# Performance work log

Hardware: AMD Instinct MI355X
Metric: run time of the kernel (lower is better)

The kernel has to match this reference:

```python
import jax, jax.numpy as jnp
import numpy as np

D_MODEL = 4096
D_FF = 11008

def _dequant_matmul(x, w_int, s):
    # x: [N, in], w_int: [out, in] int, s: [out, 1] -> [N, out]
    w = w_int.astype(jnp.float32) * s  # dequantized weight [out, in]
    return x @ w.T

def setup_inputs() -> dict:
    key = jax.random.key(0)
    ks = jax.random.split(key, 7)
    x = jax.random.normal(ks[0], (4, 2048, D_MODEL), dtype=jnp.float32)
    gate_w = jax.random.randint(ks[1], (D_FF, D_MODEL), -128, 128, dtype=jnp.int32)
    up_w = jax.random.randint(ks[2], (D_FF, D_MODEL), -128, 128, dtype=jnp.int32)
    down_w = jax.random.randint(ks[3], (D_MODEL, D_FF), -128, 128, dtype=jnp.int32)
    gate_s = jax.random.uniform(ks[4], (D_FF, 1), dtype=jnp.float32) * 0.01
    up_s = jax.random.uniform(ks[5], (D_FF, 1), dtype=jnp.float32) * 0.01
    down_s = jax.random.uniform(ks[6], (D_MODEL, 1), dtype=jnp.float32) * 0.01
    return {"x": x, "gate_w": gate_w, "gate_s": gate_s, "up_w": up_w,
            "up_s": up_s, "down_w": down_w, "down_s": down_s}

def reference(x, gate_w, gate_s, up_w, up_s, down_w, down_s):
    batch, seq_len, hidden = x.shape
    x_flat = x.reshape(-1, hidden).astype(jnp.float32)
    gate = _dequant_matmul(x_flat, gate_w, gate_s)
    up = _dequant_matmul(x_flat, up_w, up_s)
    h = jax.nn.silu(gate) * up
    out = _dequant_matmul(h, down_w, down_s)
    return out.astype(x.dtype).reshape(batch, seq_len, hidden)
```

## Files before the change

### kernel.cpp

```cpp
#include <hip/hip_runtime.h>


typedef __attribute__((ext_vector_type(8))) __bf16 bf16x8;
typedef __attribute__((ext_vector_type(4))) float f32x4;
typedef __attribute__((ext_vector_type(8))) unsigned short ushort8;
typedef __attribute__((ext_vector_type(4))) int i32x4;

#define D_MODEL 4096
#define D_FF    11008
#define NTOK    8192

static __device__ __forceinline__ unsigned short f32_to_bf16(float f) {
    union { float f; unsigned u; } v; v.f = f;
    unsigned r = v.u + 0x7fffu + ((v.u >> 16) & 1u);
    return (unsigned short)(r >> 16);
}
static __device__ __forceinline__ float bf16_to_f32(unsigned short s) {
    union { unsigned u; float f; } v; v.u = ((unsigned)s) << 16;
    return v.f;
}
static __device__ __forceinline__ void gload_lds16(const void* g, void* l) {
    __builtin_amdgcn_global_load_lds(
        (const __attribute__((address_space(1))) void*)g,
        (__attribute__((address_space(3))) void*)l, 16, 0, 0);
}

__global__ __launch_bounds__(256)
void pack_w_kernel(const int* __restrict__ w, signed char* __restrict__ out,
                   long long total)
{
    long long i = ((long long)blockIdx.x * 256 + threadIdx.x) * 8;
    if (i >= total) return;
    int4 w0 = *(const int4*)(w + i);
    int4 w1 = *(const int4*)(w + i + 4);
    union { signed char c[8]; unsigned long long u; } r;
    r.c[0] = (signed char)w0.x; r.c[1] = (signed char)w0.y;
    r.c[2] = (signed char)w0.z; r.c[3] = (signed char)w0.w;
    r.c[4] = (signed char)w1.x; r.c[5] = (signed char)w1.y;
    r.c[6] = (signed char)w1.z; r.c[7] = (signed char)w1.w;
    *(unsigned long long*)(out + i) = r.u;
}

__global__ __launch_bounds__(256)
void dequant_w_kernel(const int* __restrict__ w, const float* __restrict__ s,
                      unsigned short* __restrict__ out, int cols, long long total)
{
    long long i = ((long long)blockIdx.x * 256 + threadIdx.x) * 8;
    if (i >= total) return;
    float sc = s[(int)(i / cols)];
    int4 w0 = *(const int4*)(w + i);
    int4 w1 = *(const int4*)(w + i + 4);
    ushort8 r;
    r[0] = f32_to_bf16((float)w0.x * sc);
    r[1] = f32_to_bf16((float)w0.y * sc);
    r[2] = f32_to_bf16((float)w0.z * sc);
    r[3] = f32_to_bf16((float)w0.w * sc);
    r[4] = f32_to_bf16((float)w1.x * sc);
    r[5] = f32_to_bf16((float)w1.y * sc);
    r[6] = f32_to_bf16((float)w1.z * sc);
    r[7] = f32_to_bf16((float)w1.w * sc);
    *(ushort8*)(out + i) = r;
}

__global__ __launch_bounds__(256)
void quant_x_kernel(const float* __restrict__ x, signed char* __restrict__ xq,
                    float* __restrict__ xs)
{
    __shared__ float red[4];
    const int row = blockIdx.x;
    const int t   = threadIdx.x;
    const float* xr = x + (size_t)row * D_MODEL;
    float4 v0 = *(const float4*)(xr + t * 16);
    float4 v1 = *(const float4*)(xr + t * 16 + 4);
    float4 v2 = *(const float4*)(xr + t * 16 + 8);
    float4 v3 = *(const float4*)(xr + t * 16 + 12);
    float m = fabsf(v0.x);
    m = fmaxf(m, fabsf(v0.y)); m = fmaxf(m, fabsf(v0.z)); m = fmaxf(m, fabsf(v0.w));
    m = fmaxf(m, fabsf(v1.x)); m = fmaxf(m, fabsf(v1.y)); m = fmaxf(m, fabsf(v1.z)); m = fmaxf(m, fabsf(v1.w));
    m = fmaxf(m, fabsf(v2.x)); m = fmaxf(m, fabsf(v2.y)); m = fmaxf(m, fabsf(v2.z)); m = fmaxf(m, fabsf(v2.w));
    m = fmaxf(m, fabsf(v3.x)); m = fmaxf(m, fabsf(v3.y)); m = fmaxf(m, fabsf(v3.z)); m = fmaxf(m, fabsf(v3.w));
    #pragma unroll
    for (int o = 32; o > 0; o >>= 1) m = fmaxf(m, __shfl_xor(m, o));
    if ((t & 63) == 0) red[t >> 6] = m;
    __syncthreads();
    m = fmaxf(fmaxf(red[0], red[1]), fmaxf(red[2], red[3]));
    m = fmaxf(m, 1e-20f);
    const float inv = 127.0f / m;
    if (t == 0) xs[row] = m / 127.0f;
    union { signed char c[16]; int4 i; } r;
    #pragma unroll
    for (int j = 0; j < 4; ++j) {
        float4 v = (j == 0) ? v0 : (j == 1) ? v1 : (j == 2) ? v2 : v3;
        r.c[j*4+0] = (signed char)(int)rintf(fminf(fmaxf(v.x*inv,-127.f),127.f));
        r.c[j*4+1] = (signed char)(int)rintf(fminf(fmaxf(v.y*inv,-127.f),127.f));
        r.c[j*4+2] = (signed char)(int)rintf(fminf(fmaxf(v.z*inv,-127.f),127.f));
        r.c[j*4+3] = (signed char)(int)rintf(fminf(fmaxf(v.w*inv,-127.f),127.f));
    }
    *(int4*)(xq + (size_t)row * D_MODEL + t * 16) = r.i;
}

template<int MODE>
__global__ __launch_bounds__(512, 2)
void gemm_i8(const signed char* __restrict__ A,
             const signed char* __restrict__ B,
             unsigned short* __restrict__ C,
             const unsigned short* __restrict__ gateb,
             const float* __restrict__ xs,
             const float* __restrict__ cs,
             int M, int N, int K)
{
    extern __shared__ char smem[];
    const int tid = threadIdx.x;
    const int l   = tid & 63;
    const int w   = tid >> 6;
    const int wm  = w >> 2;
    const int wn  = w & 3;

    const int nbx  = gridDim.x;
    const int nwg  = nbx * gridDim.y;
    const int orig = blockIdx.y * nbx + blockIdx.x;
    const int cpx  = nwg >> 3;
    const int swz  = (orig & 7) * cpx + (orig >> 3);
    const int bn = swz % nbx, bm = swz / nbx;
    const int m0 = bm * 256, n0 = bn * 256;

    const int st_r = tid >> 2;
    const int st_c = ((tid & 3) ^ ((st_r >> 1) & 3)) << 4;
    const signed char* gA = A + (size_t)(m0 + st_r) * K + st_c;
    const signed char* gB = B + (size_t)(n0 + st_r) * K + st_c;
    const size_t ld128 = (size_t)128 * K;

    const int s4v = l >> 4;
    const int rA = wm * 128 + (l & 15);
    const int rB = wn * 64  + (l & 15);
    const int offA = rA * 64 + ((s4v << 4) ^ (((rA >> 1) & 3) << 4));
    const int offB = 16384 + rB * 64 + ((s4v << 4) ^ (((rB >> 1) & 3) << 4));

    i32x4 acc[8][4] = {};
    i32x4 af[4], bfr[4];

#define SBAR()  __builtin_amdgcn_sched_barrier(0)
#define BAR()   __builtin_amdgcn_s_barrier()
#define VM4()   asm volatile("s_waitcnt vmcnt(4)" ::: "memory")

#define ST_A8(SS, NXT) do { \
    const signed char* p_ = gA + ((size_t)(SS) << 6); \
    gload_lds16(p_,         smem + (NXT) + (tid & 0xFFC0 ? 0 : 0) + (w << 10)); \
    gload_lds16(p_ + ld128, smem + (NXT) + 8192 + (w << 10)); } while (0)
#define ST_B8(SS, NXT) do { \
    const signed char* p_ = gB + ((size_t)(SS) << 6); \
    gload_lds16(p_,         smem + (NXT) + 16384 + (w << 10)); \
    gload_lds16(p_ + ld128, smem + (NXT) + 16384 + 8192 + (w << 10)); } while (0)

#define MFMA16_I8(MB) do { \
    _Pragma("unroll") \
    for (int mi_ = 0; mi_ < 4; ++mi_) { \
        _Pragma("unroll") \
        for (int ni_ = 0; ni_ < 4; ++ni_) { \
            acc[(MB) + mi_][ni_] = __builtin_amdgcn_mfma_i32_16x16x64_i8( \
                af[mi_], bfr[ni_], acc[(MB) + mi_][ni_], 0, 0, 0); \
        } } } while (0)

#define STEP8(CUR, NXT, SS) do { \
    af[0]  = *(const i32x4*)(smem + (CUR) + offA); \
    af[1]  = *(const i32x4*)(smem + (CUR) + offA + 1024); \
    af[2]  = *(const i32x4*)(smem + (CUR) + offA + 2048); \
    af[3]  = *(const i32x4*)(smem + (CUR) + offA + 3072); \
    bfr[0] = *(const i32x4*)(smem + (CUR) + offB); \
    bfr[1] = *(const i32x4*)(smem + (CUR) + offB + 1024); \
    bfr[2] = *(const i32x4*)(smem + (CUR) + offB + 2048); \
    bfr[3] = *(const i32x4*)(smem + (CUR) + offB + 3072); \
    ST_A8(SS, NXT); \
    SBAR(); BAR(); \
    __builtin_amdgcn_s_setprio(1); MFMA16_I8(0); __builtin_amdgcn_s_setprio(0); \
    SBAR(); BAR(); \
    af[0] = *(const i32x4*)(smem + (CUR) + offA + 4096); \
    af[1] = *(const i32x4*)(smem + (CUR) + offA + 5120); \
    af[2] = *(const i32x4*)(smem + (CUR) + offA + 6144); \
    af[3] = *(const i32x4*)(smem + (CUR) + offA + 7168); \
    ST_B8(SS, NXT); \
    SBAR(); BAR(); \
    __builtin_amdgcn_s_setprio(1); MFMA16_I8(4); __builtin_amdgcn_s_setprio(0); \
    VM4(); SBAR(); BAR(); \
} while (0)

    ST_A8(0, 0);      ST_B8(0, 0);
    ST_A8(1, 32768);  ST_B8(1, 32768);
    VM4(); SBAR(); BAR();

    const int T = K >> 6;
    #pragma unroll 1
    for (int s = 0; s < T; s += 4) {
        int s2 = s + 2; if (s2 >= T) s2 -= T;
        int s3 = s + 3; if (s3 >= T) s3 -= T;
        int s4 = s + 4; if (s4 >= T) s4 -= T;
        int s5 = s + 5; if (s5 >= T) s5 -= T;
        STEP8(0,     65536, s2);
        STEP8(32768, 98304, s3);
        STEP8(65536, 0,     s4);
        STEP8(98304, 32768, s5);
    }
    asm volatile("s_waitcnt vmcnt(0)" ::: "memory");

    const int er = (l >> 4) * 4;
    const int ec = l & 15;
    #pragma unroll
    for (int mi = 0; mi < 8; ++mi) {
        const int rowb = m0 + wm * 128 + mi * 16 + er;
        const float4 xsv = *(const float4*)(xs + rowb);
        #pragma unroll
        for (int ni = 0; ni < 4; ++ni) {
            const int col = n0 + wn * 64 + ni * 16 + ec;
            const float csc = cs[col];
            #pragma unroll
            for (int q = 0; q < 4; ++q) {
                const int row = rowb + q;
                const float xsc = (q == 0) ? xsv.x : (q == 1) ? xsv.y
                                 : (q == 2) ? xsv.z : xsv.w;
                size_t idx = (size_t)row * N + col;
                float v = (float)acc[mi][ni][q] * csc * xsc;
                if (MODE == 0) {
                    C[idx] = f32_to_bf16(v);
                } else {
                    float g   = bf16_to_f32(gateb[idx]);
                    float sig = 1.0f / (1.0f + __expf(-g));
                    C[idx] = f32_to_bf16(g * sig * v);
                }
            }
        }
    }
#undef STEP8
#undef MFMA16_I8
#undef ST_A8
#undef ST_B8
#undef VM4
#undef BAR
#undef SBAR
}

template<int MODE>
__global__ __launch_bounds__(512, 2)
void gemm256(const unsigned short* __restrict__ A,
             const unsigned short* __restrict__ B,
             void* __restrict__ C,
             int M, int N, int K)
{
    extern __shared__ char smem[];
    const int tid = threadIdx.x;
    const int l   = tid & 63;
    const int w   = tid >> 6;
    const int wm  = w >> 2;
    const int wn  = w & 3;

    const int nbx  = gridDim.x;
    const int nwg  = nbx * gridDim.y;
    const int orig = blockIdx.y * nbx + blockIdx.x;
    const int cpx  = nwg >> 3;
    const int swz  = (orig & 7) * cpx + (orig >> 3);
    const int bn = swz % nbx, bm = swz / nbx;
    const int m0 = bm * 256, n0 = bn * 256;

    const int st_r = w * 16 + (l >> 2);
    const int st_c = (((l & 3) ^ ((l >> 3) & 3)) << 3);
    const unsigned short* gA = A + (size_t)(m0 + st_r) * K + st_c;
    const unsigned short* gB = B + (size_t)(n0 + st_r) * K + st_c;
    const size_t ld128 = (size_t)128 * K;

    const int s4v = l >> 4;
    const int rA = wm * 128 + (l & 15);
    const int rB = wn * 64  + (l & 15);
    const int offA = rA * 64 + ((s4v << 4) ^ (((rA >> 1) & 3) << 4));
    const int offB = 32768 + rB * 64 + ((s4v << 4) ^ (((rB >> 1) & 3) << 4));

    f32x4 acc[8][4] = {};
    bf16x8 af[4], bfr[4];

#define SBAR()  __builtin_amdgcn_sched_barrier(0)
#define BAR()   __builtin_amdgcn_s_barrier()
#define VM4()   asm volatile("s_waitcnt vmcnt(4)" ::: "memory")
#define STAGE2(SRC, LOFF) do { \
    gload_lds16((SRC), smem + (LOFF) + (w << 10)); \
    gload_lds16((SRC) + ld128, smem + (LOFF) + 8192 + (w << 10)); } while (0)

#define MFMA16(MB) do { \
    _Pragma("unroll") \
    for (int mi_ = 0; mi_ < 4; ++mi_) { \
        _Pragma("unroll") \
        for (int ni_ = 0; ni_ < 4; ++ni_) { \
            acc[(MB) + mi_][ni_] = __builtin_amdgcn_mfma_f32_16x16x32_bf16( \
                af[mi_], bfr[ni_], acc[(MB) + mi_][ni_], 0, 0, 0); \
        } } } while (0)

#define TILE(DB, KTN) do { \
    const int CB = (DB) * 65536; \
    const int PB = ((DB) ^ 1) * 65536; \
    const unsigned short* sA = gA + ((size_t)(KTN) << 6); \
    const unsigned short* sB = gB + ((size_t)(KTN) << 6); \
    af[0]  = *(const bf16x8*)(smem + CB + offA); \
    af[1]  = *(const bf16x8*)(smem + CB + offA + 1024); \
    af[2]  = *(const bf16x8*)(smem + CB + offA + 2048); \
    af[3]  = *(const bf16x8*)(smem + CB + offA + 3072); \
    bfr[0] = *(const bf16x8*)(smem + CB + offB); \
    bfr[1] = *(const bf16x8*)(smem + CB + offB + 1024); \
    bfr[2] = *(const bf16x8*)(smem + CB + offB + 2048); \
    bfr[3] = *(const bf16x8*)(smem + CB + offB + 3072); \
    STAGE2(sA, PB); \
    SBAR(); BAR(); \
    __builtin_amdgcn_s_setprio(1); MFMA16(0); __builtin_amdgcn_s_setprio(0); \
    SBAR(); BAR(); \
    af[0] = *(const bf16x8*)(smem + CB + offA + 4096); \
    af[1] = *(const bf16x8*)(smem + CB + offA + 5120); \
    af[2] = *(const bf16x8*)(smem + CB + offA + 6144); \
    af[3] = *(const bf16x8*)(smem + CB + offA + 7168); \
    STAGE2(sB, PB + 32768); \
    SBAR(); BAR(); \
    __builtin_amdgcn_s_setprio(1); MFMA16(4); __builtin_amdgcn_s_setprio(0); \
    VM4(); SBAR(); BAR(); \
    af[0]  = *(const bf16x8*)(smem + CB + 16384 + offA); \
    af[1]  = *(const bf16x8*)(smem + CB + 16384 + offA + 1024); \
    af[2]  = *(const bf16x8*)(smem + CB + 16384 + offA + 2048); \
    af[3]  = *(const bf16x8*)(smem + CB + 16384 + offA + 3072); \
    bfr[0] = *(const bf16x8*)(smem + CB + 16384 + offB); \
    bfr[1] = *(const bf16x8*)(smem + CB + 16384 + offB + 1024); \
    bfr[2] = *(const bf16x8*)(smem + CB + 16384 + offB + 2048); \
    bfr[3] = *(const bf16x8*)(smem + CB + 16384 + offB + 3072); \
    STAGE2(sA + 32, PB + 16384); \
    SBAR(); BAR(); \
    __builtin_amdgcn_s_setprio(1); MFMA16(0); __builtin_amdgcn_s_setprio(0); \
    SBAR(); BAR(); \
    af[0] = *(const bf16x8*)(smem + CB + 16384 + offA + 4096); \
    af[1] = *(const bf16x8*)(smem + CB + 16384 + offA + 5120); \
    af[2] = *(const bf16x8*)(smem + CB + 16384 + offA + 6144); \
    af[3] = *(const bf16x8*)(smem + CB + 16384 + offA + 7168); \
    STAGE2(sB + 32, PB + 49152); \
    SBAR(); BAR(); \
    __builtin_amdgcn_s_setprio(1); MFMA16(4); __builtin_amdgcn_s_setprio(0); \
    VM4(); SBAR(); BAR(); \
} while (0)

    STAGE2(gA,      0);
    STAGE2(gB,      32768);
    STAGE2(gA + 32, 16384);
    STAGE2(gB + 32, 49152);
    VM4(); SBAR(); BAR();

    const int T = K >> 6;
    const int T2 = T >> 1;
    #pragma unroll 1
    for (int it = 0; it < T2; ++it) {
        const int t0 = it << 1;
        TILE(0, t0 + 1);
        const int kt2 = (t0 + 2 == T) ? 0 : (t0 + 2);
        TILE(1, kt2);
    }
    asm volatile("s_waitcnt vmcnt(0)" ::: "memory");

    const int er = (l >> 4) * 4;
    const int ec = l & 15;
    #pragma unroll
    for (int mi = 0; mi < 8; ++mi) {
        #pragma unroll
        for (int ni = 0; ni < 4; ++ni) {
            #pragma unroll
            for (int q = 0; q < 4; ++q) {
                int row = m0 + wm * 128 + mi * 16 + er + q;
                int col = n0 + wn * 64  + ni * 16 + ec;
                size_t idx = (size_t)row * N + col;
                float v = acc[mi][ni][q];
                if (MODE == 0) ((unsigned short*)C)[idx] = f32_to_bf16(v);
                else           ((float*)C)[idx] = v;
            }
        }
    }
#undef TILE
#undef MFMA16
#undef STAGE2
#undef VM4
#undef BAR
#undef SBAR
}

extern "C" void kernel_launch(void* const* d_in, const int* in_sizes, int n_in,
                              void* d_out, int out_size, void* d_ws, size_t ws_size,
                              hipStream_t stream)
{
    const float* x  = (const float*)d_in[0];
    const int*   gw = (const int*)  d_in[1];
    const float* gs = (const float*)d_in[2];
    const int*   uw = (const int*)  d_in[3];
    const float* us = (const float*)d_in[4];
    const int*   dw = (const int*)  d_in[5];
    const float* dsc= (const float*)d_in[6];

    char* ws = (char*)d_ws;
    signed char*    Xq  = (signed char*)ws;    ws += (size_t)NTOK * D_MODEL;
    float*          xs  = (float*)ws;          ws += (size_t)NTOK * 4;
    signed char*    Wg8 = (signed char*)ws;    ws += (size_t)D_FF * D_MODEL;
    signed char*    Wu8 = (signed char*)ws;    ws += (size_t)D_FF * D_MODEL;
    unsigned short* Wd  = (unsigned short*)ws; ws += (size_t)D_MODEL * D_FF * 2;
    unsigned short* H   = (unsigned short*)ws;

    const long long wtot = (long long)D_FF * D_MODEL;

    hipFuncSetAttribute(reinterpret_cast<const void*>(gemm_i8<0>),
                        hipFuncAttributeMaxDynamicSharedMemorySize, 131072);
    hipFuncSetAttribute(reinterpret_cast<const void*>(gemm_i8<1>),
                        hipFuncAttributeMaxDynamicSharedMemorySize, 131072);
    hipFuncSetAttribute(reinterpret_cast<const void*>(gemm256<2>),
                        hipFuncAttributeMaxDynamicSharedMemorySize, 131072);

    pack_w_kernel   <<<(int)(wtot / 2048), 256, 0, stream>>>(gw, Wg8, wtot);
    pack_w_kernel   <<<(int)(wtot / 2048), 256, 0, stream>>>(uw, Wu8, wtot);
    dequant_w_kernel<<<(int)(wtot / 2048), 256, 0, stream>>>(dw, dsc, Wd, D_FF, wtot);
    quant_x_kernel  <<<NTOK, 256, 0, stream>>>(x, Xq, xs);

    dim3 g1(D_FF / 256, NTOK / 256);
    gemm_i8<0><<<g1, 512, 131072, stream>>>(Xq, Wg8, H, nullptr, xs, gs,
                                            NTOK, D_FF, D_MODEL);
    gemm_i8<1><<<g1, 512, 131072, stream>>>(Xq, Wu8, H, H, xs, us,
                                            NTOK, D_FF, D_MODEL);
    dim3 g3(D_MODEL / 256, NTOK / 256);
    gemm256<2><<<g3, 512, 131072, stream>>>(H, Wd, d_out, NTOK, D_MODEL, D_FF);
}
```

Before: 1.651 ms.

## Fuse gate and up int8 GEMMs via interleaved weight packing

```diff
diff --git a/kernel.cpp b/kernel.cpp
--- a/kernel.cpp
+++ b/kernel.cpp
@@ -15,10 +15,6 @@
     unsigned r = v.u + 0x7fffu + ((v.u >> 16) & 1u);
     return (unsigned short)(r >> 16);
 }
-static __device__ __forceinline__ float bf16_to_f32(unsigned short s) {
-    union { unsigned u; float f; } v; v.u = ((unsigned)s) << 16;
-    return v.f;
-}
 static __device__ __forceinline__ void gload_lds16(const void* g, void* l) {
     __builtin_amdgcn_global_load_lds(
         (const __attribute__((address_space(1))) void*)g,
@@ -26,19 +22,23 @@
 }
 
 __global__ __launch_bounds__(256)
-void pack_w_kernel(const int* __restrict__ w, signed char* __restrict__ out,
-                   long long total)
+void pack_gu_kernel(const int* __restrict__ gw, const int* __restrict__ uw,
+                    signed char* __restrict__ out)
 {
     long long i = ((long long)blockIdx.x * 256 + threadIdx.x) * 8;
-    if (i >= total) return;
-    int4 w0 = *(const int4*)(w + i);
-    int4 w1 = *(const int4*)(w + i + 4);
-    union { signed char c[8]; unsigned long long u; } r;
-    r.c[0] = (signed char)w0.x; r.c[1] = (signed char)w0.y;
-    r.c[2] = (signed char)w0.z; r.c[3] = (signed char)w0.w;
-    r.c[4] = (signed char)w1.x; r.c[5] = (signed char)w1.y;
-    r.c[6] = (signed char)w1.z; r.c[7] = (signed char)w1.w;
-    *(unsigned long long*)(out + i) = r.u;
+    const int r = (int)(i >> 12);
+    const int k = (int)(i & 4095);
+    const int src_row = ((r >> 5) << 4) + (r & 15);
+    const int* src = ((r >> 4) & 1) ? uw : gw;
+    const int* p = src + (size_t)src_row * D_MODEL + k;
+    int4 w0 = *(const int4*)(p);
+    int4 w1 = *(const int4*)(p + 4);
+    union { signed char c[8]; unsigned long long u; } rr;
+    rr.c[0] = (signed char)w0.x; rr.c[1] = (signed char)w0.y;
+    rr.c[2] = (signed char)w0.z; rr.c[3] = (signed char)w0.w;
+    rr.c[4] = (signed char)w1.x; rr.c[5] = (signed char)w1.y;
+    rr.c[6] = (signed char)w1.z; rr.c[7] = (signed char)w1.w;
+    *(unsigned long long*)(out + i) = rr.u;
 }
 
 __global__ __launch_bounds__(256)
@@ -99,15 +99,14 @@
     *(int4*)(xq + (size_t)row * D_MODEL + t * 16) = r.i;
 }
 
-template<int MODE>
 __global__ __launch_bounds__(512, 2)
-void gemm_i8(const signed char* __restrict__ A,
-             const signed char* __restrict__ B,
-             unsigned short* __restrict__ C,
-             const unsigned short* __restrict__ gateb,
-             const float* __restrict__ xs,
-             const float* __restrict__ cs,
-             int M, int N, int K)
+void gemm_i8gu(const signed char* __restrict__ A,
+               const signed char* __restrict__ B,
+               unsigned short* __restrict__ H,
+               const float* __restrict__ xs,
+               const float* __restrict__ gs,
+               const float* __restrict__ us,
+               int M, int NH, int K)
 {
     extern __shared__ char smem[];
     const int tid = threadIdx.x;
@@ -145,7 +144,7 @@
 
 #define ST_A8(SS, NXT) do { \
     const signed char* p_ = gA + ((size_t)(SS) << 6); \
-    gload_lds16(p_,         smem + (NXT) + (tid & 0xFFC0 ? 0 : 0) + (w << 10)); \
+    gload_lds16(p_,         smem + (NXT) + (w << 10)); \
     gload_lds16(p_ + ld128, smem + (NXT) + 8192 + (w << 10)); } while (0)
 #define ST_B8(SS, NXT) do { \
     const signed char* p_ = gB + ((size_t)(SS) << 6); \
@@ -204,28 +203,24 @@
 
     const int er = (l >> 4) * 4;
     const int ec = l & 15;
+    const int hbase = (n0 >> 1) + wn * 32;
     #pragma unroll
     for (int mi = 0; mi < 8; ++mi) {
         const int rowb = m0 + wm * 128 + mi * 16 + er;
         const float4 xsv = *(const float4*)(xs + rowb);
         #pragma unroll
-        for (int ni = 0; ni < 4; ++ni) {
-            const int col = n0 + wn * 64 + ni * 16 + ec;
-            const float csc = cs[col];
+        for (int p = 0; p < 2; ++p) {
+            const int c = hbase + p * 16 + ec;
+            const float sg = gs[c];
+            const float su = us[c];
             #pragma unroll
             for (int q = 0; q < 4; ++q) {
-                const int row = rowb + q;
                 const float xsc = (q == 0) ? xsv.x : (q == 1) ? xsv.y
                                  : (q == 2) ? xsv.z : xsv.w;
-                size_t idx = (size_t)row * N + col;
-                float v = (float)acc[mi][ni][q] * csc * xsc;
-                if (MODE == 0) {
-                    C[idx] = f32_to_bf16(v);
-                } else {
-                    float g   = bf16_to_f32(gateb[idx]);
-                    float sig = 1.0f / (1.0f + __expf(-g));
-                    C[idx] = f32_to_bf16(g * sig * v);
-                }
+                float g = (float)acc[mi][2*p][q]     * sg * xsc;
+                float u = (float)acc[mi][2*p + 1][q] * su * xsc;
+                float sig = 1.0f / (1.0f + __expf(-g));
+                H[(size_t)(rowb + q) * NH + c] = f32_to_bf16(g * sig * u);
             }
         }
     }
@@ -238,12 +233,11 @@
 #undef SBAR
 }
 
-template<int MODE>
 __global__ __launch_bounds__(512, 2)
-void gemm256(const unsigned short* __restrict__ A,
-             const unsigned short* __restrict__ B,
-             void* __restrict__ C,
-             int M, int N, int K)
+void gemm256_down(const unsigned short* __restrict__ A,
+                  const unsigned short* __restrict__ B,
+                  float* __restrict__ C,
+                  int M, int N, int K)
 {
     extern __shared__ char smem[];
     const int tid = threadIdx.x;
@@ -365,10 +359,7 @@
             for (int q = 0; q < 4; ++q) {
                 int row = m0 + wm * 128 + mi * 16 + er + q;
                 int col = n0 + wn * 64  + ni * 16 + ec;
-                size_t idx = (size_t)row * N + col;
-                float v = acc[mi][ni][q];
-                if (MODE == 0) ((unsigned short*)C)[idx] = f32_to_bf16(v);
-                else           ((float*)C)[idx] = v;
+                C[(size_t)row * N + col] = acc[mi][ni][q];
             }
         }
     }
@@ -393,32 +384,29 @@
     const float* dsc= (const float*)d_in[6];
 
     char* ws = (char*)d_ws;
-    signed char*    Xq  = (signed char*)ws;    ws += (size_t)NTOK * D_MODEL;
-    float*          xs  = (float*)ws;          ws += (size_t)NTOK * 4;
-    signed char*    Wg8 = (signed char*)ws;    ws += (size_t)D_FF * D_MODEL;
-    signed char*    Wu8 = (signed char*)ws;    ws += (size_t)D_FF * D_MODEL;
-    unsigned short* Wd  = (unsigned short*)ws; ws += (size_t)D_MODEL * D_FF * 2;
-    unsigned short* H   = (unsigned short*)ws;
-
-    const long long wtot = (long long)D_FF * D_MODEL;
-
-    hipFuncSetAttribute(reinterpret_cast<const void*>(gemm_i8<0>),
+    signed char*    Xq   = (signed char*)ws;    ws += (size_t)NTOK * D_MODEL;
+    float*          xs   = (float*)ws;          ws += (size_t)NTOK * 4;
+    signed char*    Wgu8 = (signed char*)ws;    ws += (size_t)2 * D_FF * D_MODEL;
+    unsigned short* Wd   = (unsigned short*)ws; ws += (size_t)D_MODEL * D_FF * 2;
+    unsigned short* H    = (unsigned short*)ws;
+
+    const long long wtot  = (long long)D_FF * D_MODEL;
+    const long long gutot = 2LL * wtot;
+
+    hipFuncSetAttribute(reinterpret_cast<const void*>(gemm_i8gu),
                         hipFuncAttributeMaxDynamicSharedMemorySize, 131072);
-    hipFuncSetAttribute(reinterpret_cast<const void*>(gemm_i8<1>),
+    hipFuncSetAttribute(reinterpret_cast<const void*>(gemm256_down),
                         hipFuncAttributeMaxDynamicSharedMemorySize, 131072);
-    hipFuncSetAttribute(reinterpret_cast<const void*>(gemm256<2>),
-                        hipFuncAttributeMaxDynamicSharedMemorySize, 131072);
-
-    pack_w_kernel   <<<(int)(wtot / 2048), 256, 0, stream>>>(gw, Wg8, wtot);
-    pack_w_kernel   <<<(int)(wtot / 2048), 256, 0, stream>>>(uw, Wu8, wtot);
-    dequant_w_kernel<<<(int)(wtot / 2048), 256, 0, stream>>>(dw, dsc, Wd, D_FF, wtot);
+
+    pack_gu_kernel  <<<(int)(gutot / 2048), 256, 0, stream>>>(gw, uw, Wgu8);
+    dequant_w_kernel<<<(int)(wtot  / 2048), 256, 0, stream>>>(dw, dsc, Wd, D_FF, wtot);
     quant_x_kernel  <<<NTOK, 256, 0, stream>>>(x, Xq, xs);
 
-    dim3 g1(D_FF / 256, NTOK / 256);
-    gemm_i8<0><<<g1, 512, 131072, stream>>>(Xq, Wg8, H, nullptr, xs, gs,
-                                            NTOK, D_FF, D_MODEL);
-    gemm_i8<1><<<g1, 512, 131072, stream>>>(Xq, Wu8, H, H, xs, us,
-                                            NTOK, D_FF, D_MODEL);
+    dim3 g1(2 * D_FF / 256, NTOK / 256);
+    gemm_i8gu<<<g1, 512, 131072, stream>>>(Xq, Wgu8, H, xs, gs, us,
+                                           NTOK, D_FF, D_MODEL);
+
     dim3 g3(D_MODEL / 256, NTOK / 256);
-    gemm256<2><<<g3, 512, 131072, stream>>>(H, Wd, d_out, NTOK, D_MODEL, D_FF);
-}
+    gemm256_down<<<g3, 512, 131072, stream>>>(H, Wd, (float*)d_out,
+                                              NTOK, D_MODEL, D_FF);
+}
```

Measured after the change: 1.539 ms. 6.8% less time.
